# Performance work log

Hardware: AMD Instinct MI355X
Metric: run time of the kernel (lower is better)

The kernel has to match this reference:

```python
import jax, jax.numpy as jnp
import numpy as np

L = 4      # num_layers
H = 8      # nhead
D = 128    # d_model
FF = 256   # dim_feedforward
V = 16     # vocab_size
S = 1024   # window_size (== seq_len, mask is built at this size)
B = 8      # batch
LW = 128   # local attention window (+- LW)
EPS = 1e-5 # torch LayerNorm default


def setup_inputs() -> dict:
    key = jax.random.key(0)
    ks = jax.random.split(key, 8)
    n = lambda k, shape, s=0.02: jax.random.normal(k, shape, dtype=jnp.float32) * s
    return {
        "token_batch": jax.random.randint(ks[0], (B, S), 0, V, dtype=jnp.int32),
        "emb": n(ks[1], (V, D), 1.0),
        "Wqkv": n(ks[2], (L, 3 * D, D)), "bqkv": jnp.zeros((L, 3 * D)),
        "Wo": n(ks[3], (L, D, D)), "bo": jnp.zeros((L, D)),
        "ln1_g": jnp.ones((L, D)), "ln1_b": jnp.zeros((L, D)),
        "ln2_g": jnp.ones((L, D)), "ln2_b": jnp.zeros((L, D)),
        "W1": n(ks[4], (L, FF, D)), "b1": jnp.zeros((L, FF)),
        "W2": n(ks[5], (L, D, FF)), "b2": jnp.zeros((L, D)),
        "lnf_g": jnp.ones((D,)), "lnf_b": jnp.zeros((D,)),
        "Wout": n(ks[6], (1, D)), "bout": jnp.zeros((1,)),
    }


def _ln(x, g, b):
    m = jnp.mean(x, axis=-1, keepdims=True)
    v = jnp.var(x, axis=-1, keepdims=True)
    return (x - m) / jnp.sqrt(v + EPS) * g + b


def _pos_encoding(seq_len, d_model):
    pos = jnp.arange(seq_len, dtype=jnp.float32)[:, None]
    div = jnp.exp(jnp.arange(0, d_model, 2, dtype=jnp.float32) * (-jnp.log(10000.0) / d_model))
    pe = jnp.zeros((seq_len, d_model), dtype=jnp.float32)
    pe = pe.at[:, 0::2].set(jnp.sin(pos * div))
    pe = pe.at[:, 1::2].set(jnp.cos(pos * div))
    return pe


def reference(token_batch, emb, Wqkv, bqkv, Wo, bo, ln1_g, ln1_b, ln2_g, ln2_b,
              W1, b1, W2, b2, lnf_g, lnf_b, Wout, bout):
    Bn, Sn = token_batch.shape
    Dm = emb.shape[1]
    hd = Dm // H
    # embedding + sinusoidal positions (dropout is identity in eval mode)
    x = emb[token_batch] + _pos_encoding(Sn, Dm)[None]  # [B,S,D]
    # local band mask: 0 inside +-LW, -inf outside (as in _create_local_attention_mask)
    i = jnp.arange(Sn)
    mask = jnp.where(jnp.abs(i[:, None] - i[None, :]) <= LW, 0.0, -jnp.inf)  # [S,S]
    for l in range(Wqkv.shape[0]):
        # post-norm TransformerEncoderLayer, relu activation (torch defaults)
        qkv = x @ Wqkv[l].T + bqkv[l]
        q, k, v = jnp.split(qkv, 3, axis=-1)
        q = q.reshape(Bn, Sn, H, hd)
        k = k.reshape(Bn, Sn, H, hd)
        v = v.reshape(Bn, Sn, H, hd)
        scores = jnp.einsum('bqhd,bkhd->bhqk', q, k) / jnp.sqrt(jnp.float32(hd)) + mask
        attn = jax.nn.softmax(scores, axis=-1)
        ctx = jnp.einsum('bhqk,bkhd->bqhd', attn, v).reshape(Bn, Sn, Dm)
        x = _ln(x + ctx @ Wo[l].T + bo[l], ln1_g[l], ln1_b[l])
        ff = jax.nn.relu(x @ W1[l].T + b1[l]) @ W2[l].T + b2[l]
        x = _ln(x + ff, ln2_g[l], ln2_b[l])
    x = _ln(x, lnf_g, lnf_b)
    out = jax.nn.softplus(x @ Wout.T + bout)  # [B,S,1]
    return out[..., 0]
```

## Files before the change

kernel.cpp:

```cpp
#include <hip/hip_runtime.h>
#include <hip/hip_bf16.h>
#include <math.h>

#define NL   4
#define NH   8
#define DM   128
#define FFD  256
#define SEQ  1024
#define BATCH 8
#define NT   (BATCH*SEQ)
#define EPSV 1e-5f

typedef _Float16 h16;
typedef h16   h16x8 __attribute__((ext_vector_type(8)));
typedef float f32x4 __attribute__((ext_vector_type(4)));

#define WQKV_OFF 0
#define WO_OFF   196608
#define W1_OFF   262144
#define W2_OFF   393216
#define WTOT     524288

__global__ __launch_bounds__(256) void prep_kernel(
    const int* __restrict__ tok, const float* __restrict__ emb,
    float* __restrict__ x, h16* __restrict__ xh,
    const float* __restrict__ wqkv, const float* __restrict__ wo,
    const float* __restrict__ w1, const float* __restrict__ w2,
    h16* __restrict__ wdst)
{
    int bid = blockIdx.x;
    if (bid < 4096) {
        int idx = bid * 256 + threadIdx.x;
        int t = idx >> 7;
        int d = idx & 127;
        int s = t & (SEQ - 1);
        int token = tok[t];
        float freq = expf((float)(d & ~1) * (-9.210340371976184f / 128.0f));
        float ang = (float)s * freq;
        float pe = (d & 1) ? cosf(ang) : sinf(ang);
        float v = emb[token * DM + d] + pe;
        x[idx] = v;
        xh[idx] = (h16)v;
    } else {
        int i = ((bid - 4096) * 256 + threadIdx.x) * 4;
        const float* src; int off;
        if (i < WO_OFF)      { src = wqkv; off = 0; }
        else if (i < W1_OFF) { src = wo;   off = WO_OFF; }
        else if (i < W2_OFF) { src = w1;   off = W1_OFF; }
        else                 { src = w2;   off = W2_OFF; }
        float4 v = *(const float4*)&src[i - off];
        h16 o[4] = {(h16)v.x, (h16)v.y, (h16)v.z, (h16)v.w};
        *(uint2*)&wdst[i] = *(uint2*)o;
    }
}

__global__ __launch_bounds__(256) void gemm16_kernel(
    const h16* __restrict__ A, const h16* __restrict__ W,
    const float* __restrict__ bias, h16* __restrict__ out16, int N)
{
    __shared__ h16 Al[64 * 136];
    __shared__ h16 Wl[64 * 136];

    int tid = threadIdx.x;
    long row0 = (long)blockIdx.x * 64;
    long col0 = (long)blockIdx.y * 64;

    for (int idx = tid; idx < 64 * 16; idx += 256) {
        int r = idx >> 4, c = idx & 15;
        *(uint4*)&Al[r * 136 + c * 8] = *(const uint4*)&A[(row0 + r) * 128 + c * 8];
        *(uint4*)&Wl[r * 136 + c * 8] = *(const uint4*)&W[(col0 + r) * 128 + c * 8];
    }
    __syncthreads();

    int lane = tid & 63, wv = tid >> 6;
    int lr = lane & 15, lg = lane >> 4;
    int wr = (wv >> 1) * 32, wc = (wv & 1) * 32;

    f32x4 acc[2][2] = {{{0.f,0.f,0.f,0.f},{0.f,0.f,0.f,0.f}},
                       {{0.f,0.f,0.f,0.f},{0.f,0.f,0.f,0.f}}};

    #pragma unroll
    for (int k0 = 0; k0 < 128; k0 += 32) {
        h16x8 a0 = *(const h16x8*)&Al[(wr +      lr) * 136 + k0 + lg * 8];
        h16x8 a1 = *(const h16x8*)&Al[(wr + 16 + lr) * 136 + k0 + lg * 8];
        h16x8 b0 = *(const h16x8*)&Wl[(wc +      lr) * 136 + k0 + lg * 8];
        h16x8 b1 = *(const h16x8*)&Wl[(wc + 16 + lr) * 136 + k0 + lg * 8];
        acc[0][0] = __builtin_amdgcn_mfma_f32_16x16x32_f16(a0, b0, acc[0][0], 0, 0, 0);
        acc[0][1] = __builtin_amdgcn_mfma_f32_16x16x32_f16(a0, b1, acc[0][1], 0, 0, 0);
        acc[1][0] = __builtin_amdgcn_mfma_f32_16x16x32_f16(a1, b0, acc[1][0], 0, 0, 0);
        acc[1][1] = __builtin_amdgcn_mfma_f32_16x16x32_f16(a1, b1, acc[1][1], 0, 0, 0);
    }

    #pragma unroll
    for (int m = 0; m < 2; ++m)
    #pragma unroll
    for (int n = 0; n < 2; ++n) {
        long col = col0 + wc + 16 * n + lr;
        float bv = bias[col];
        #pragma unroll
        for (int r = 0; r < 4; ++r) {
            long row = row0 + wr + 16 * m + lg * 4 + r;
            out16[row * N + col] = (h16)(acc[m][n][r] + bv);
        }
    }
}

#define NSLOT 336
#define KSTR  24
#define VSTR  344
#define PSTR  296

__global__ __launch_bounds__(256) void attn16_kernel(
    const h16* __restrict__ qkvh, h16* __restrict__ ctxh)
{
    __shared__ h16 Kl[NSLOT * KSTR];
    __shared__ h16 Vt[16 * VSTR];
    __shared__ h16 Pl[4 * 16 * PSTR];

    int tid = threadIdx.x;
    int blk = blockIdx.x;
    int qb = blk & 15;
    int h  = (blk >> 4) & 7;
    int b  = blk >> 7;
    int q0b = qb * 64;
    int kw0 = q0b - 128;

    for (int idx = tid; idx < NSLOT * 2; idx += 256) {
        int slot = idx >> 1, part = (idx & 1) * 8;
        int ka = kw0 + slot;
        uint4 val = {0u, 0u, 0u, 0u};
        if (ka >= 0 && ka < SEQ)
            val = *(const uint4*)&qkvh[((size_t)(b * SEQ + ka)) * 384 + h * 16 + 128 + part];
        *(uint4*)&Kl[slot * KSTR + part] = val;
    }
    for (int idx = tid; idx < NSLOT * 2; idx += 256) {
        int slot = idx >> 1, part = (idx & 1) * 8;
        int ka = kw0 + slot;
        uint4 val = {0u, 0u, 0u, 0u};
        if (ka >= 0 && ka < SEQ)
            val = *(const uint4*)&qkvh[((size_t)(b * SEQ + ka)) * 384 + h * 16 + 256 + part];
        h16 tmp[8];
        *(uint4*)tmp = val;
        #pragma unroll
        for (int j = 0; j < 8; ++j)
            Vt[(part + j) * VSTR + slot] = tmp[j];
    }
    __syncthreads();

    int lane = tid & 63, w = tid >> 6;
    int lr = lane & 15, lg = lane >> 4;
    int q0w = q0b + w * 16;

    h16x8 qf = {0, 0, 0, 0, 0, 0, 0, 0};
    if (lg < 2)
        qf = *(const h16x8*)&qkvh[((size_t)(b * SEQ + q0w + lr)) * 384 + h * 16 + lg * 8];
    qf = qf * (h16)0.25f;

    f32x4 s[17];
    const f32x4 zero4 = {0.f, 0.f, 0.f, 0.f};
    #pragma unroll
    for (int t = 0; t < 17; ++t) {
        h16x8 kf = {0, 0, 0, 0, 0, 0, 0, 0};
        if (lg < 2)
            kf = *(const h16x8*)&Kl[(w * 16 + t * 16 + lr) * KSTR + lg * 8];
        s[t] = __builtin_amdgcn_mfma_f32_16x16x32_f16(qf, kf, zero4, 0, 0, 0);
    }

    bool interior = (q0b >= 128) && (q0b <= 832);
    if (interior) {
        #pragma unroll
        for (int r = 0; r < 4; ++r) {
            int qr = lg * 4 + r;
            if (lr < qr) s[0][r]  = -1e30f;
            if (lr > qr) s[16][r] = -1e30f;
        }
    } else {
        #pragma unroll
        for (int t = 0; t < 17; ++t)
        #pragma unroll
        for (int r = 0; r < 4; ++r) {
            int rel = 16 * t + lr - (lg * 4 + r);
            int ka  = kw0 + w * 16 + 16 * t + lr;
            bool valid = (rel >= 0) && (rel <= 256) && (ka >= 0) && (ka < SEQ);
            if (!valid) s[t][r] = -1e30f;
        }
    }

    float mx[4] = {-1e30f, -1e30f, -1e30f, -1e30f};
    #pragma unroll
    for (int t = 0; t < 17; ++t)
        #pragma unroll
        for (int r = 0; r < 4; ++r) mx[r] = fmaxf(mx[r], s[t][r]);
    #pragma unroll
    for (int r = 0; r < 4; ++r) {
        mx[r] = fmaxf(mx[r], __shfl_xor(mx[r], 1));
        mx[r] = fmaxf(mx[r], __shfl_xor(mx[r], 2));
        mx[r] = fmaxf(mx[r], __shfl_xor(mx[r], 4));
        mx[r] = fmaxf(mx[r], __shfl_xor(mx[r], 8));
    }
    float sum[4] = {0.f, 0.f, 0.f, 0.f};
    #pragma unroll
    for (int t = 0; t < 17; ++t)
        #pragma unroll
        for (int r = 0; r < 4; ++r) {
            float p = __expf(s[t][r] - mx[r]);
            s[t][r] = p;
            sum[r] += p;
        }
    #pragma unroll
    for (int r = 0; r < 4; ++r) {
        sum[r] += __shfl_xor(sum[r], 1);
        sum[r] += __shfl_xor(sum[r], 2);
        sum[r] += __shfl_xor(sum[r], 4);
        sum[r] += __shfl_xor(sum[r], 8);
    }

    h16* Pw = &Pl[w * 16 * PSTR];
    #pragma unroll
    for (int t = 0; t < 17; ++t)
        #pragma unroll
        for (int r = 0; r < 4; ++r)
            Pw[(lg * 4 + r) * PSTR + t * 16 + lr] = (h16)s[t][r];
    #pragma unroll
    for (int r = 0; r < 4; ++r)
        Pw[(lg * 4 + r) * PSTR + 272 + lr] = (h16)0.f;

    f32x4 o = {0.f, 0.f, 0.f, 0.f};
    #pragma unroll
    for (int c = 0; c < 9; ++c) {
        h16x8 pf = *(const h16x8*)&Pw[lr * PSTR + c * 32 + lg * 8];
        h16x8 vf = *(const h16x8*)&Vt[lr * VSTR + w * 16 + c * 32 + lg * 8];
        o = __builtin_amdgcn_mfma_f32_16x16x32_f16(pf, vf, o, 0, 0, 0);
    }

    #pragma unroll
    for (int r = 0; r < 4; ++r) {
        float val = o[r] / sum[r];
        ctxh[((size_t)(b * SEQ + q0w + lg * 4 + r)) * DM + h * 16 + lr] = (h16)val;
    }
}

template<int LAST>
__global__ __launch_bounds__(256) void tail_kernel(
    const h16* __restrict__ ctx, const float* __restrict__ xres,
    const h16* __restrict__ Wo, const float* __restrict__ bo,
    const float* __restrict__ g1, const float* __restrict__ bb1,
    const h16* __restrict__ W1, const float* __restrict__ b1,
    const h16* __restrict__ W2, const float* __restrict__ b2,
    const float* __restrict__ g2, const float* __restrict__ bb2,
    const float* __restrict__ gf, const float* __restrict__ bf,
    const float* __restrict__ Wout, const float* __restrict__ bout,
    float* __restrict__ x_out, h16* __restrict__ xh_out,
    float* __restrict__ out)
{
    __shared__ h16 Xl[32 * 136];
    __shared__ h16 Wl[128 * 136];
    __shared__ h16 Al[32 * 136];
    __shared__ float red[32][2][2];

    int tid = threadIdx.x;
    long row0 = (long)blockIdx.x * 32;

    for (int idx = tid; idx < 32 * 16; idx += 256) {
        int r = idx >> 4, c = idx & 15;
        *(uint4*)&Xl[r * 136 + c * 8] = *(const uint4*)&ctx[(row0 + r) * 128 + c * 8];
    }
    for (int idx = tid; idx < 128 * 16; idx += 256) {
        int r = idx >> 4, c = idx & 15;
        *(uint4*)&Wl[r * 136 + c * 8] = *(const uint4*)&Wo[r * 128 + c * 8];
    }
    __syncthreads();

    int lane = tid & 63, w = tid >> 6;
    int lr = lane & 15, lg = lane >> 4;
    int wrow = (w >> 1) * 16, wcol = (w & 1) * 64;
    int cg = w & 1;

    f32x4 acc[4] = {{0.f,0.f,0.f,0.f},{0.f,0.f,0.f,0.f},
                    {0.f,0.f,0.f,0.f},{0.f,0.f,0.f,0.f}};
    #pragma unroll
    for (int k0 = 0; k0 < 128; k0 += 32) {
        h16x8 af = *(const h16x8*)&Xl[(wrow + lr) * 136 + k0 + lg * 8];
        #pragma unroll
        for (int n = 0; n < 4; ++n) {
            h16x8 bfr = *(const h16x8*)&Wl[(wcol + 16 * n + lr) * 136 + k0 + lg * 8];
            acc[n] = __builtin_amdgcn_mfma_f32_16x16x32_f16(af, bfr, acc[n], 0, 0, 0);
        }
    }

    float val1[4][4];
    #pragma unroll
    for (int r = 0; r < 4; ++r) {
        long row = row0 + wrow + lg * 4 + r;
        #pragma unroll
        for (int n = 0; n < 4; ++n) {
            int col = wcol + 16 * n + lr;
            val1[r][n] = acc[n][r] + bo[col] + xres[row * 128 + col];
        }
    }
    #pragma unroll
    for (int r = 0; r < 4; ++r) {
        float s  = val1[r][0] + val1[r][1] + val1[r][2] + val1[r][3];
        float sq = val1[r][0]*val1[r][0] + val1[r][1]*val1[r][1]
                 + val1[r][2]*val1[r][2] + val1[r][3]*val1[r][3];
        #pragma unroll
        for (int m = 1; m < 16; m <<= 1) {
            s  += __shfl_xor(s, m);
            sq += __shfl_xor(sq, m);
        }
        if (lr == 0) {
            red[wrow + lg * 4 + r][cg][0] = s;
            red[wrow + lg * 4 + r][cg][1] = sq;
        }
    }
    __syncthreads();
    #pragma unroll
    for (int r = 0; r < 4; ++r) {
        int rowt = wrow + lg * 4 + r;
        float S  = red[rowt][0][0] + red[rowt][1][0];
        float SQ = red[rowt][0][1] + red[rowt][1][1];
        float mean = S * (1.0f / 128.0f);
        float var  = SQ * (1.0f / 128.0f) - mean * mean;
        float rstd = rsqrtf(var + EPSV);
        #pragma unroll
        for (int n = 0; n < 4; ++n) {
            int col = wcol + 16 * n + lr;
            val1[r][n] = (val1[r][n] - mean) * rstd * g1[col] + bb1[col];
        }
    }
    #pragma unroll
    for (int r = 0; r < 4; ++r)
        #pragma unroll
        for (int n = 0; n < 4; ++n)
            Xl[(wrow + lg * 4 + r) * 136 + wcol + 16 * n + lr] = (h16)val1[r][n];

    f32x4 acc2[4] = {{0.f,0.f,0.f,0.f},{0.f,0.f,0.f,0.f},
                     {0.f,0.f,0.f,0.f},{0.f,0.f,0.f,0.f}};

    #pragma unroll 1
    for (int half = 0; half < 2; ++half) {
        for (int idx = tid; idx < 128 * 16; idx += 256) {
            int r = idx >> 4, c = idx & 15;
            *(uint4*)&Wl[r * 136 + c * 8] =
                *(const uint4*)&W1[(long)(128 * half + r) * 128 + c * 8];
        }
        __syncthreads();

        f32x4 a1[4] = {{0.f,0.f,0.f,0.f},{0.f,0.f,0.f,0.f},
                       {0.f,0.f,0.f,0.f},{0.f,0.f,0.f,0.f}};
        #pragma unroll
        for (int k0 = 0; k0 < 128; k0 += 32) {
            h16x8 af = *(const h16x8*)&Xl[(wrow + lr) * 136 + k0 + lg * 8];
            #pragma unroll
            for (int n = 0; n < 4; ++n) {
                h16x8 bfr = *(const h16x8*)&Wl[(wcol + 16 * n + lr) * 136 + k0 + lg * 8];
                a1[n] = __builtin_amdgcn_mfma_f32_16x16x32_f16(af, bfr, a1[n], 0, 0, 0);
            }
        }
        __syncthreads();

        #pragma unroll
        for (int r = 0; r < 4; ++r)
            #pragma unroll
            for (int n = 0; n < 4; ++n) {
                int col = wcol + 16 * n + lr;
                float v = a1[n][r] + b1[128 * half + col];
                Al[(wrow + lg * 4 + r) * 136 + col] = (h16)fmaxf(v, 0.f);
            }
        for (int idx = tid; idx < 128 * 16; idx += 256) {
            int r = idx >> 4, c = idx & 15;
            *(uint4*)&Wl[r * 136 + c * 8] =
                *(const uint4*)&W2[(long)r * 256 + 128 * half + c * 8];
        }
        __syncthreads();

        #pragma unroll
        for (int k0 = 0; k0 < 128; k0 += 32) {
            h16x8 af = *(const h16x8*)&Al[(wrow + lr) * 136 + k0 + lg * 8];
            #pragma unroll
            for (int n = 0; n < 4; ++n) {
                h16x8 bfr = *(const h16x8*)&Wl[(wcol + 16 * n + lr) * 136 + k0 + lg * 8];
                acc2[n] = __builtin_amdgcn_mfma_f32_16x16x32_f16(af, bfr, acc2[n], 0, 0, 0);
            }
        }
        __syncthreads();
    }

    float val2[4][4];
    #pragma unroll
    for (int r = 0; r < 4; ++r)
        #pragma unroll
        for (int n = 0; n < 4; ++n) {
            int col = wcol + 16 * n + lr;
            val2[r][n] = acc2[n][r] + b2[col] + val1[r][n];
        }
    #pragma unroll
    for (int r = 0; r < 4; ++r) {
        float s  = val2[r][0] + val2[r][1] + val2[r][2] + val2[r][3];
        float sq = val2[r][0]*val2[r][0] + val2[r][1]*val2[r][1]
                 + val2[r][2]*val2[r][2] + val2[r][3]*val2[r][3];
        #pragma unroll
        for (int m = 1; m < 16; m <<= 1) {
            s  += __shfl_xor(s, m);
            sq += __shfl_xor(sq, m);
        }
        if (lr == 0) {
            red[wrow + lg * 4 + r][cg][0] = s;
            red[wrow + lg * 4 + r][cg][1] = sq;
        }
    }
    __syncthreads();
    #pragma unroll
    for (int r = 0; r < 4; ++r) {
        int rowt = wrow + lg * 4 + r;
        float S  = red[rowt][0][0] + red[rowt][1][0];
        float SQ = red[rowt][0][1] + red[rowt][1][1];
        float mean = S * (1.0f / 128.0f);
        float var  = SQ * (1.0f / 128.0f) - mean * mean;
        float rstd = rsqrtf(var + EPSV);
        #pragma unroll
        for (int n = 0; n < 4; ++n) {
            int col = wcol + 16 * n + lr;
            val2[r][n] = (val2[r][n] - mean) * rstd * g2[col] + bb2[col];
        }
    }

    if (!LAST) {
        #pragma unroll
        for (int r = 0; r < 4; ++r) {
            long row = row0 + wrow + lg * 4 + r;
            #pragma unroll
            for (int n = 0; n < 4; ++n) {
                int col = wcol + 16 * n + lr;
                x_out[row * 128 + col]  = val2[r][n];
                xh_out[row * 128 + col] = (h16)val2[r][n];
            }
        }
    } else {
        __syncthreads();
        #pragma unroll
        for (int r = 0; r < 4; ++r) {
            float s  = val2[r][0] + val2[r][1] + val2[r][2] + val2[r][3];
            float sq = val2[r][0]*val2[r][0] + val2[r][1]*val2[r][1]
                     + val2[r][2]*val2[r][2] + val2[r][3]*val2[r][3];
            #pragma unroll
            for (int m = 1; m < 16; m <<= 1) {
                s  += __shfl_xor(s, m);
                sq += __shfl_xor(sq, m);
            }
            if (lr == 0) {
                red[wrow + lg * 4 + r][cg][0] = s;
                red[wrow + lg * 4 + r][cg][1] = sq;
            }
        }
        __syncthreads();
        float dotp[4];
        #pragma unroll
        for (int r = 0; r < 4; ++r) {
            int rowt = wrow + lg * 4 + r;
            float S  = red[rowt][0][0] + red[rowt][1][0];
            float SQ = red[rowt][0][1] + red[rowt][1][1];
            float mean = S * (1.0f / 128.0f);
            float var  = SQ * (1.0f / 128.0f) - mean * mean;
            float rstd = rsqrtf(var + EPSV);
            float d = 0.f;
            #pragma unroll
            for (int n = 0; n < 4; ++n) {
                int col = wcol + 16 * n + lr;
                float nf = (val2[r][n] - mean) * rstd * gf[col] + bf[col];
                d = fmaf(nf, Wout[col], d);
            }
            #pragma unroll
            for (int m = 1; m < 16; m <<= 1) d += __shfl_xor(d, m);
            dotp[r] = d;
        }
        __syncthreads();
        #pragma unroll
        for (int r = 0; r < 4; ++r)
            if (lr == 0) red[wrow + lg * 4 + r][cg][0] = dotp[r];
        __syncthreads();
        if (tid < 32) {
            float z = red[tid][0][0] + red[tid][1][0] + bout[0];
            out[row0 + tid] = fmaxf(z, 0.f) + log1pf(__expf(-fabsf(z)));
        }
    }
}

extern "C" void kernel_launch(void* const* d_in, const int* in_sizes, int n_in,
                              void* d_out, int out_size, void* d_ws, size_t ws_size,
                              hipStream_t stream)
{
    const int*   tok  = (const int*)d_in[0];
    const float* emb  = (const float*)d_in[1];
    const float* Wqkv = (const float*)d_in[2];
    const float* bqkv = (const float*)d_in[3];
    const float* Wo   = (const float*)d_in[4];
    const float* bo   = (const float*)d_in[5];
    const float* ln1g = (const float*)d_in[6];
    const float* ln1b = (const float*)d_in[7];
    const float* ln2g = (const float*)d_in[8];
    const float* ln2b = (const float*)d_in[9];
    const float* W1   = (const float*)d_in[10];
    const float* b1   = (const float*)d_in[11];
    const float* W2   = (const float*)d_in[12];
    const float* b2   = (const float*)d_in[13];
    const float* lnfg = (const float*)d_in[14];
    const float* lnfb = (const float*)d_in[15];
    const float* Wout = (const float*)d_in[16];
    const float* bout = (const float*)d_in[17];
    float* out = (float*)d_out;

    char* wsb = (char*)d_ws;
    float* x    = (float*)wsb;
    h16*   xh   = (h16*)(wsb + 4194304);
    h16*   qkvh = (h16*)(wsb + 6291456);
    h16*   ctxh = (h16*)(wsb + 12582912);
    h16*   wh   = (h16*)(wsb + 14680064);

    h16* Wqkv_h = wh + WQKV_OFF;
    h16* Wo_h   = wh + WO_OFF;
    h16* W1_h   = wh + W1_OFF;
    h16* W2_h   = wh + W2_OFF;

    prep_kernel<<<4096 + WTOT / 1024, 256, 0, stream>>>(
        tok, emb, x, xh, Wqkv, Wo, W1, W2, wh);

    for (int l = 0; l < NL; ++l) {
        gemm16_kernel<<<dim3(NT / 64, 384 / 64), 256, 0, stream>>>(
            xh, Wqkv_h + (size_t)l * 384 * 128, bqkv + l * 384, qkvh, 384);
        attn16_kernel<<<BATCH * NH * (SEQ / 64), 256, 0, stream>>>(qkvh, ctxh);
        if (l < NL - 1) {
            tail_kernel<0><<<NT / 32, 256, 0, stream>>>(
                ctxh, x,
                Wo_h + (size_t)l * 128 * 128, bo + l * 128,
                ln1g + l * DM, ln1b + l * DM,
                W1_h + (size_t)l * 256 * 128, b1 + l * 256,
                W2_h + (size_t)l * 128 * 256, b2 + l * 128,
                ln2g + l * DM, ln2b + l * DM,
                lnfg, lnfb, Wout, bout,
                x, xh, out);
        } else {
            tail_kernel<1><<<NT / 32, 256, 0, stream>>>(
                ctxh, x,
                Wo_h + (size_t)l * 128 * 128, bo + l * 128,
                ln1g + l * DM, ln1b + l * DM,
                W1_h + (size_t)l * 256 * 128, b1 + l * 256,
                W2_h + (size_t)l * 128 * 256, b2 + l * 128,
                ln2g + l * DM, ln2b + l * DM,
                lnfg, lnfb, Wout, bout,
                x, xh, out);
        }
    }
}
```

Measured before the change: 245.1 us.

## Double-buffer weight staging in tail kernel with 512 threads; split attention P buffer

The fused tail kernel now runs 512 threads (8 waves, each owning a 16x32 output tile) and uses two LDS weight buffers, so the next weight slice (W1 halves, W2 halves) is loaded while the current GEMM runs. This removes some barrier-bound serial load/compute phases. The attention kernel writes its probability tile in two smaller chunks, shrinking the per-wave P scratch roughly in half, which lowers LDS use and may allow more resident blocks. The tail kernel's LDS grows by a second 128x136 buffer, and the doubled thread count may cut occupancy per CU.

Measured after the change: 225.7 us. 1.09x faster.

```diff
diff --git a/kernel.cpp b/kernel.cpp
--- a/kernel.cpp
+++ b/kernel.cpp
@@ -108,14 +108,14 @@
 #define NSLOT 336
 #define KSTR  24
 #define VSTR  344
-#define PSTR  296
+#define PSTR2 168
 
 __global__ __launch_bounds__(256) void attn16_kernel(
     const h16* __restrict__ qkvh, h16* __restrict__ ctxh)
 {
     __shared__ h16 Kl[NSLOT * KSTR];
     __shared__ h16 Vt[16 * VSTR];
-    __shared__ h16 Pl[4 * 16 * PSTR];
+    __shared__ h16 Pl[4 * 16 * PSTR2];
 
     int tid = threadIdx.x;
     int blk = blockIdx.x;
@@ -215,23 +215,34 @@
         sum[r] += __shfl_xor(sum[r], 8);
     }
 
-    h16* Pw = &Pl[w * 16 * PSTR];
-    #pragma unroll
-    for (int t = 0; t < 17; ++t)
+    h16* Pw = &Pl[w * 16 * PSTR2];
+    f32x4 o = {0.f, 0.f, 0.f, 0.f};
+
+    #pragma unroll
+    for (int t = 0; t < 10; ++t)
         #pragma unroll
         for (int r = 0; r < 4; ++r)
-            Pw[(lg * 4 + r) * PSTR + t * 16 + lr] = (h16)s[t][r];
-    #pragma unroll
-    for (int r = 0; r < 4; ++r)
-        Pw[(lg * 4 + r) * PSTR + 272 + lr] = (h16)0.f;
-
-    f32x4 o = {0.f, 0.f, 0.f, 0.f};
-    #pragma unroll
-    for (int c = 0; c < 9; ++c) {
-        h16x8 pf = *(const h16x8*)&Pw[lr * PSTR + c * 32 + lg * 8];
+            Pw[(lg * 4 + r) * PSTR2 + t * 16 + lr] = (h16)s[t][r];
+    #pragma unroll
+    for (int c = 0; c < 5; ++c) {
+        h16x8 pf = *(const h16x8*)&Pw[lr * PSTR2 + c * 32 + lg * 8];
         h16x8 vf = *(const h16x8*)&Vt[lr * VSTR + w * 16 + c * 32 + lg * 8];
         o = __builtin_amdgcn_mfma_f32_16x16x32_f16(pf, vf, o, 0, 0, 0);
     }
+    #pragma unroll
+    for (int t = 10; t < 17; ++t)
+        #pragma unroll
+        for (int r = 0; r < 4; ++r)
+            Pw[(lg * 4 + r) * PSTR2 + (t - 10) * 16 + lr] = (h16)s[t][r];
+    #pragma unroll
+    for (int r = 0; r < 4; ++r)
+        Pw[(lg * 4 + r) * PSTR2 + 112 + lr] = (h16)0.f;
+    #pragma unroll
+    for (int c = 0; c < 4; ++c) {
+        h16x8 pf = *(const h16x8*)&Pw[lr * PSTR2 + c * 32 + lg * 8];
+        h16x8 vf = *(const h16x8*)&Vt[lr * VSTR + w * 16 + (c + 5) * 32 + lg * 8];
+        o = __builtin_amdgcn_mfma_f32_16x16x32_f16(pf, vf, o, 0, 0, 0);
+    }
 
     #pragma unroll
     for (int r = 0; r < 4; ++r) {
@@ -241,7 +252,7 @@
 }
 
 template<int LAST>
-__global__ __launch_bounds__(256) void tail_kernel(
+__global__ __launch_bounds__(512) void tail_kernel(
     const h16* __restrict__ ctx, const float* __restrict__ xres,
     const h16* __restrict__ Wo, const float* __restrict__ bo,
     const float* __restrict__ g1, const float* __restrict__ bb1,
@@ -254,55 +265,60 @@
     float* __restrict__ out)
 {
     __shared__ h16 Xl[32 * 136];
-    __shared__ h16 Wl[128 * 136];
+    __shared__ h16 Wl[2][128 * 136];
     __shared__ h16 Al[32 * 136];
-    __shared__ float red[32][2][2];
+    __shared__ float red[32][4][2];
 
     int tid = threadIdx.x;
     long row0 = (long)blockIdx.x * 32;
-
-    for (int idx = tid; idx < 32 * 16; idx += 256) {
-        int r = idx >> 4, c = idx & 15;
-        *(uint4*)&Xl[r * 136 + c * 8] = *(const uint4*)&ctx[(row0 + r) * 128 + c * 8];
-    }
-    for (int idx = tid; idx < 128 * 16; idx += 256) {
-        int r = idx >> 4, c = idx & 15;
-        *(uint4*)&Wl[r * 136 + c * 8] = *(const uint4*)&Wo[r * 128 + c * 8];
-    }
-    __syncthreads();
-
     int lane = tid & 63, w = tid >> 6;
     int lr = lane & 15, lg = lane >> 4;
-    int wrow = (w >> 1) * 16, wcol = (w & 1) * 64;
-    int cg = w & 1;
-
-    f32x4 acc[4] = {{0.f,0.f,0.f,0.f},{0.f,0.f,0.f,0.f},
-                    {0.f,0.f,0.f,0.f},{0.f,0.f,0.f,0.f}};
+    int wrow = (w >> 2) * 16;
+    int wcol = (w & 3) * 32;
+    int cg = w & 3;
+
+    auto stageW = [&](int buf, const h16* src, long rstride, long roff, long coff) {
+        #pragma unroll
+        for (int it = 0; it < 4; ++it) {
+            int idx = tid + it * 512;
+            int r = idx >> 4, c = idx & 15;
+            *(uint4*)&Wl[buf][r * 136 + c * 8] =
+                *(const uint4*)&src[(roff + r) * rstride + coff + c * 8];
+        }
+    };
+
+    {
+        int r = tid >> 4, c = tid & 15;
+        *(uint4*)&Xl[r * 136 + c * 8] = *(const uint4*)&ctx[(row0 + r) * 128 + c * 8];
+    }
+    stageW(0, Wo, 128, 0, 0);
+    __syncthreads();
+
+    stageW(1, W1, 128, 0, 0);
+    f32x4 acc[2] = {{0.f,0.f,0.f,0.f},{0.f,0.f,0.f,0.f}};
     #pragma unroll
     for (int k0 = 0; k0 < 128; k0 += 32) {
         h16x8 af = *(const h16x8*)&Xl[(wrow + lr) * 136 + k0 + lg * 8];
         #pragma unroll
-        for (int n = 0; n < 4; ++n) {
-            h16x8 bfr = *(const h16x8*)&Wl[(wcol + 16 * n + lr) * 136 + k0 + lg * 8];
+        for (int n = 0; n < 2; ++n) {
+            h16x8 bfr = *(const h16x8*)&Wl[0][(wcol + 16 * n + lr) * 136 + k0 + lg * 8];
             acc[n] = __builtin_amdgcn_mfma_f32_16x16x32_f16(af, bfr, acc[n], 0, 0, 0);
         }
     }
-
-    float val1[4][4];
+    float val1[4][2];
     #pragma unroll
     for (int r = 0; r < 4; ++r) {
         long row = row0 + wrow + lg * 4 + r;
         #pragma unroll
-        for (int n = 0; n < 4; ++n) {
+        for (int n = 0; n < 2; ++n) {
             int col = wcol + 16 * n + lr;
             val1[r][n] = acc[n][r] + bo[col] + xres[row * 128 + col];
         }
     }
     #pragma unroll
     for (int r = 0; r < 4; ++r) {
-        float s  = val1[r][0] + val1[r][1] + val1[r][2] + val1[r][3];
-        float sq = val1[r][0]*val1[r][0] + val1[r][1]*val1[r][1]
-                 + val1[r][2]*val1[r][2] + val1[r][3]*val1[r][3];
+        float s  = val1[r][0] + val1[r][1];
+        float sq = val1[r][0]*val1[r][0] + val1[r][1]*val1[r][1];
         #pragma unroll
         for (int m = 1; m < 16; m <<= 1) {
             s  += __shfl_xor(s, m);
@@ -314,91 +330,101 @@
         }
     }
     __syncthreads();
+
+    stageW(0, W2, 256, 0, 0);
     #pragma unroll
     for (int r = 0; r < 4; ++r) {
         int rowt = wrow + lg * 4 + r;
-        float S  = red[rowt][0][0] + red[rowt][1][0];
-        float SQ = red[rowt][0][1] + red[rowt][1][1];
+        float S  = red[rowt][0][0] + red[rowt][1][0] + red[rowt][2][0] + red[rowt][3][0];
+        float SQ = red[rowt][0][1] + red[rowt][1][1] + red[rowt][2][1] + red[rowt][3][1];
         float mean = S * (1.0f / 128.0f);
         float var  = SQ * (1.0f / 128.0f) - mean * mean;
         float rstd = rsqrtf(var + EPSV);
         #pragma unroll
-        for (int n = 0; n < 4; ++n) {
+        for (int n = 0; n < 2; ++n) {
             int col = wcol + 16 * n + lr;
             val1[r][n] = (val1[r][n] - mean) * rstd * g1[col] + bb1[col];
+            Xl[rowt * 136 + col] = (h16)val1[r][n];
+        }
+    }
+    __syncthreads();
+
+    f32x4 a1[2] = {{0.f,0.f,0.f,0.f},{0.f,0.f,0.f,0.f}};
+    #pragma unroll
+    for (int k0 = 0; k0 < 128; k0 += 32) {
+        h16x8 af = *(const h16x8*)&Xl[(wrow + lr) * 136 + k0 + lg * 8];
+        #pragma unroll
+        for (int n = 0; n < 2; ++n) {
+            h16x8 bfr = *(const h16x8*)&Wl[1][(wcol + 16 * n + lr) * 136 + k0 + lg * 8];
+            a1[n] = __builtin_amdgcn_mfma_f32_16x16x32_f16(af, bfr, a1[n], 0, 0, 0);
         }
     }
     #pragma unroll
     for (int r = 0; r < 4; ++r)
         #pragma unroll
-        for (int n = 0; n < 4; ++n)
-            Xl[(wrow + lg * 4 + r) * 136 + wcol + 16 * n + lr] = (h16)val1[r][n];
-
-    f32x4 acc2[4] = {{0.f,0.f,0.f,0.f},{0.f,0.f,0.f,0.f},
-                     {0.f,0.f,0.f,0.f},{0.f,0.f,0.f,0.f}};
-
-    #pragma unroll 1
-    for (int half = 0; half < 2; ++half) {
-        for (int idx = tid; idx < 128 * 16; idx += 256) {
-            int r = idx >> 4, c = idx & 15;
-            *(uint4*)&Wl[r * 136 + c * 8] =
-                *(const uint4*)&W1[(long)(128 * half + r) * 128 + c * 8];
-        }
-        __syncthreads();
-
-        f32x4 a1[4] = {{0.f,0.f,0.f,0.f},{0.f,0.f,0.f,0.f},
-                       {0.f,0.f,0.f,0.f},{0.f,0.f,0.f,0.f}};
-        #pragma unroll
-        for (int k0 = 0; k0 < 128; k0 += 32) {
-            h16x8 af = *(const h16x8*)&Xl[(wrow + lr) * 136 + k0 + lg * 8];
-            #pragma unroll
-            for (int n = 0; n < 4; ++n) {
-                h16x8 bfr = *(const h16x8*)&Wl[(wcol + 16 * n + lr) * 136 + k0 + lg * 8];
-                a1[n] = __builtin_amdgcn_mfma_f32_16x16x32_f16(af, bfr, a1[n], 0, 0, 0);
-            }
-        }
-        __syncthreads();
-
-        #pragma unroll
-        for (int r = 0; r < 4; ++r)
-            #pragma unroll
-            for (int n = 0; n < 4; ++n) {
-                int col = wcol + 16 * n + lr;
-                float v = a1[n][r] + b1[128 * half + col];
-                Al[(wrow + lg * 4 + r) * 136 + col] = (h16)fmaxf(v, 0.f);
-            }
-        for (int idx = tid; idx < 128 * 16; idx += 256) {
-            int r = idx >> 4, c = idx & 15;
-            *(uint4*)&Wl[r * 136 + c * 8] =
-                *(const uint4*)&W2[(long)r * 256 + 128 * half + c * 8];
-        }
-        __syncthreads();
-
-        #pragma unroll
-        for (int k0 = 0; k0 < 128; k0 += 32) {
-            h16x8 af = *(const h16x8*)&Al[(wrow + lr) * 136 + k0 + lg * 8];
-            #pragma unroll
-            for (int n = 0; n < 4; ++n) {
-                h16x8 bfr = *(const h16x8*)&Wl[(wcol + 16 * n + lr) * 136 + k0 + lg * 8];
-                acc2[n] = __builtin_amdgcn_mfma_f32_16x16x32_f16(af, bfr, acc2[n], 0, 0, 0);
-            }
-        }
-        __syncthreads();
-    }
-
-    float val2[4][4];
+        for (int n = 0; n < 2; ++n) {
+            int col = wcol + 16 * n + lr;
+            float v = a1[n][r] + b1[col];
+            Al[(wrow + lg * 4 + r) * 136 + col] = (h16)fmaxf(v, 0.f);
+        }
+    __syncthreads();
+
+    stageW(1, W1, 128, 128, 0);
+    f32x4 acc2[2] = {{0.f,0.f,0.f,0.f},{0.f,0.f,0.f,0.f}};
+    #pragma unroll
+    for (int k0 = 0; k0 < 128; k0 += 32) {
+        h16x8 af = *(const h16x8*)&Al[(wrow + lr) * 136 + k0 + lg * 8];
+        #pragma unroll
+        for (int n = 0; n < 2; ++n) {
+            h16x8 bfr = *(const h16x8*)&Wl[0][(wcol + 16 * n + lr) * 136 + k0 + lg * 8];
+            acc2[n] = __builtin_amdgcn_mfma_f32_16x16x32_f16(af, bfr, acc2[n], 0, 0, 0);
+        }
+    }
+    __syncthreads();
+
+    stageW(0, W2, 256, 0, 128);
+    #pragma unroll
+    for (int n = 0; n < 2; ++n) a1[n] = f32x4{0.f,0.f,0.f,0.f};
+    #pragma unroll
+    for (int k0 = 0; k0 < 128; k0 += 32) {
+        h16x8 af = *(const h16x8*)&Xl[(wrow + lr) * 136 + k0 + lg * 8];
+        #pragma unroll
+        for (int n = 0; n < 2; ++n) {
+            h16x8 bfr = *(const h16x8*)&Wl[1][(wcol + 16 * n + lr) * 136 + k0 + lg * 8];
+            a1[n] = __builtin_amdgcn_mfma_f32_16x16x32_f16(af, bfr, a1[n], 0, 0, 0);
+        }
+    }
     #pragma unroll
     for (int r = 0; r < 4; ++r)
         #pragma unroll
-        for (int n = 0; n < 4; ++n) {
+        for (int n = 0; n < 2; ++n) {
+            int col = wcol + 16 * n + lr;
+            float v = a1[n][r] + b1[128 + col];
+            Al[(wrow + lg * 4 + r) * 136 + col] = (h16)fmaxf(v, 0.f);
+        }
+    __syncthreads();
+
+    #pragma unroll
+    for (int k0 = 0; k0 < 128; k0 += 32) {
+        h16x8 af = *(const h16x8*)&Al[(wrow + lr) * 136 + k0 + lg * 8];
+        #pragma unroll
+        for (int n = 0; n < 2; ++n) {
+            h16x8 bfr = *(const h16x8*)&Wl[0][(wcol + 16 * n + lr) * 136 + k0 + lg * 8];
+            acc2[n] = __builtin_amdgcn_mfma_f32_16x16x32_f16(af, bfr, acc2[n], 0, 0, 0);
+        }
+    }
+    float val2[4][2];
+    #pragma unroll
+    for (int r = 0; r < 4; ++r)
+        #pragma unroll
+        for (int n = 0; n < 2; ++n) {
             int col = wcol + 16 * n + lr;
             val2[r][n] = acc2[n][r] + b2[col] + val1[r][n];
         }
     #pragma unroll
     for (int r = 0; r < 4; ++r) {
-        float s  = val2[r][0] + val2[r][1] + val2[r][2] + val2[r][3];
-        float sq = val2[r][0]*val2[r][0] + val2[r][1]*val2[r][1]
-                 + val2[r][2]*val2[r][2] + val2[r][3]*val2[r][3];
+        float s  = val2[r][0] + val2[r][1];
+        float sq = val2[r][0]*val2[r][0] + val2[r][1]*val2[r][1];
         #pragma unroll
         for (int m = 1; m < 16; m <<= 1) {
             s  += __shfl_xor(s, m);
@@ -410,16 +436,17 @@
         }
     }
     __syncthreads();
+
     #pragma unroll
     for (int r = 0; r < 4; ++r) {
         int rowt = wrow + lg * 4 + r;
-        float S  = red[rowt][0][0] + red[rowt][1][0];
-        float SQ = red[rowt][0][1] + red[rowt][1][1];
+        float S  = red[rowt][0][0] + red[rowt][1][0] + red[rowt][2][0] + red[rowt][3][0];
+        float SQ = red[rowt][0][1] + red[rowt][1][1] + red[rowt][2][1] + red[rowt][3][1];
         float mean = S * (1.0f / 128.0f);
         float var  = SQ * (1.0f / 128.0f) - mean * mean;
         float rstd = rsqrtf(var + EPSV);
         #pragma unroll
-        for (int n = 0; n < 4; ++n) {
+        for (int n = 0; n < 2; ++n) {
             int col = wcol + 16 * n + lr;
             val2[r][n] = (val2[r][n] - mean) * rstd * g2[col] + bb2[col];
         }
@@ -430,7 +457,7 @@
         for (int r = 0; r < 4; ++r) {
             long row = row0 + wrow + lg * 4 + r;
             #pragma unroll
-            for (int n = 0; n < 4; ++n) {
+            for (int n = 0; n < 2; ++n) {
                 int col = wcol + 16 * n + lr;
                 x_out[row * 128 + col]  = val2[r][n];
                 xh_out[row * 128 + col] = (h16)val2[r][n];
@@ -440,9 +467,8 @@
         __syncthreads();
         #pragma unroll
         for (int r = 0; r < 4; ++r) {
-            float s  = val2[r][0] + val2[r][1] + val2[r][2] + val2[r][3];
-            float sq = val2[r][0]*val2[r][0] + val2[r][1]*val2[r][1]
-                     + val2[r][2]*val2[r][2] + val2[r][3]*val2[r][3];
+            float s  = val2[r][0] + val2[r][1];
+            float sq = val2[r][0]*val2[r][0] + val2[r][1]*val2[r][1];
             #pragma unroll
             for (int m = 1; m < 16; m <<= 1) {
                 s  += __shfl_xor(s, m);
@@ -458,14 +484,14 @@
         #pragma unroll
         for (int r = 0; r < 4; ++r) {
             int rowt = wrow + lg * 4 + r;
-            float S  = red[rowt][0][0] + red[rowt][1][0];
-            float SQ = red[rowt][0][1] + red[rowt][1][1];
+            float S  = red[rowt][0][0] + red[rowt][1][0] + red[rowt][2][0] + red[rowt][3][0];
+            float SQ = red[rowt][0][1] + red[rowt][1][1] + red[rowt][2][1] + red[rowt][3][1];
             float mean = S * (1.0f / 128.0f);
             float var  = SQ * (1.0f / 128.0f) - mean * mean;
             float rstd = rsqrtf(var + EPSV);
             float d = 0.f;
             #pragma unroll
-            for (int n = 0; n < 4; ++n) {
+            for (int n = 0; n < 2; ++n) {
                 int col = wcol + 16 * n + lr;
                 float nf = (val2[r][n] - mean) * rstd * gf[col] + bf[col];
                 d = fmaf(nf, Wout[col], d);
@@ -480,7 +506,7 @@
             if (lr == 0) red[wrow + lg * 4 + r][cg][0] = dotp[r];
         __syncthreads();
         if (tid < 32) {
-            float z = red[tid][0][0] + red[tid][1][0] + bout[0];
+            float z = red[tid][0][0] + red[tid][1][0] + red[tid][2][0] + red[tid][3][0] + bout[0];
             out[row0 + tid] = fmaxf(z, 0.f) + log1pf(__expf(-fabsf(z)));
         }
     }
@@ -530,7 +556,7 @@
             xh, Wqkv_h + (size_t)l * 384 * 128, bqkv + l * 384, qkvh, 384);
         attn16_kernel<<<BATCH * NH * (SEQ / 64), 256, 0, stream>>>(qkvh, ctxh);
         if (l < NL - 1) {
-            tail_kernel<0><<<NT / 32, 256, 0, stream>>>(
+            tail_kernel<0><<<NT / 32, 512, 0, stream>>>(
                 ctxh, x,
                 Wo_h + (size_t)l * 128 * 128, bo + l * 128,
                 ln1g + l * DM, ln1b + l * DM,
@@ -540,7 +566,7 @@
                 lnfg, lnfb, Wout, bout,
                 x, xh, out);
         } else {
-            tail_kernel<1><<<NT / 32, 256, 0, stream>>>(
+            tail_kernel<1><<<NT / 32, 512, 0, stream>>>(
                 ctxh, x,
                 Wo_h + (size_t)l * 128 * 128, bo + l * 128,
                 ln1g + l * DM, ln1b + l * DM,
```
